# Kernel optimization log

Measured on AMD Instinct MI355X. Metric: run time of the kernel, lower is better.

Reference implementation:

```python
import jax, jax.numpy as jnp
import numpy as np

EMBED_DIM = 200
INPUT_DIM = 512


def setup_inputs() -> dict:
    key = jax.random.key(0)
    k1, k2, k3, k4 = jax.random.split(key, 4)
    B, L, T = 64, 256, 64
    x = jax.random.normal(k1, (B, L, INPUT_DIM), dtype=jnp.float32)
    y = jax.random.normal(k2, (B, T, INPUT_DIM), dtype=jnp.float32)
    # fc = nn.Linear(input_dim, embedding_dim)
    W = jax.random.normal(k3, (EMBED_DIM, INPUT_DIM), dtype=jnp.float32) * (1.0 / np.sqrt(INPUT_DIM))
    b = jax.random.normal(k4, (EMBED_DIM,), dtype=jnp.float32) * 0.01
    return {"x": x, "y": y, "W": W, "b": b}


def reference(x, y, W, b):
    # Project both modalities (last dim != embedding_dim in original triggers fc)
    xp = jnp.einsum('bld,ed->ble', x, W) + b   # B x L x E
    yp = jnp.einsum('btd,ed->bte', y, W) + b   # B x T x E
    # Pairwise matchmap: for pair (i, j), matchmap = xp[i] @ yp[j].T -> L x T
    mm = jnp.einsum('ile,jte->ijlt', xp, yp)   # B x B x L x T
    # MISA: max over L (rows of matchmap, dim 0), then mean over T
    S = jnp.max(mm, axis=2).mean(axis=2)       # B x B
    return S
```

## Files before the change

### kernel.cpp

```cpp
#include <hip/hip_runtime.h>
#include <hip/hip_bf16.h>
#include <stdint.h>

#define BB 64
#define LL 256
#define TT 64
#define DD 512
#define EE 200
#define EP 208
#define NKK 13
#define NROWS_X 16384
#define BSTRIDE 264

typedef __attribute__((ext_vector_type(8))) short short8;
typedef __attribute__((ext_vector_type(4))) float floatx4;
typedef __attribute__((ext_vector_type(16))) float floatx16;

__device__ __forceinline__ short f2bf(float f) {
  uint32_t u = __builtin_bit_cast(uint32_t, f);
  u = (u + 0x7fffu + ((u >> 16) & 1u)) >> 16;
  return (short)u;
}

__device__ __forceinline__ uint32_t pack2(float lo, float hi) {
  return __builtin_amdgcn_perm(__builtin_bit_cast(uint32_t, hi),
                               __builtin_bit_cast(uint32_t, lo), 0x07060302u);
}

typedef const __attribute__((address_space(1))) uint32_t gu32_t;
typedef __attribute__((address_space(3))) uint32_t lu32_t;
__device__ __forceinline__ void glds16(const void* g, void* l) {
  __builtin_amdgcn_global_load_lds((gu32_t*)g, (lu32_t*)l, 16, 0, 0);
}

__global__ void wcvt_kernel(const float* __restrict__ W, short* __restrict__ Wb) {
  const int t = blockIdx.x * 256 + threadIdx.x;
  const int base = t * 8;
  const int e = base >> 9;
  short8 o;
  if (e < EE) {
    const floatx4 f0 = *(const floatx4*)(W + base);
    const floatx4 f1 = *(const floatx4*)(W + base + 4);
    o[0] = f2bf(f0.x); o[1] = f2bf(f0.y); o[2] = f2bf(f0.z); o[3] = f2bf(f0.w);
    o[4] = f2bf(f1.x); o[5] = f2bf(f1.y); o[6] = f2bf(f1.z); o[7] = f2bf(f1.w);
  } else {
    o = (short8)0;
  }
  *(short8*)(Wb + base) = o;
}

__global__ __launch_bounds__(256, 3) void proj_kernel(const float* __restrict__ x,
                                                      const float* __restrict__ y,
                                                      const short* __restrict__ Wb,
                                                      const float* __restrict__ bias,
                                                      short* __restrict__ pT) {
  __shared__ __align__(16) char smem[43008];
  float* ldsA = (float*)smem;
  short* ldsB = (short*)(smem + 16384);
  short* bounce = (short*)smem;

  const int tid  = threadIdx.x;
  const int lane = tid & 63;
  const int wid  = tid >> 6;
  const int r16   = lane & 15;
  const int khalf = lane >> 4;

  const int row0 = blockIdx.x * 64;
  const float* srcbase = (row0 < NROWS_X) ? (x + (size_t)row0 * DD)
                                          : (y + (size_t)(row0 - NROWS_X) * DD);

  floatx4 acc[NKK];
#pragma unroll
  for (int n = 0; n < NKK; n++) acc[n] = (floatx4){0.f, 0.f, 0.f, 0.f};

  auto stage = [&](int buf, int ks) {
#pragma unroll
    for (int it = 0; it < 2; it++) {
      const int p = it * 256 + tid;
      const int r = p >> 3, c = p & 7;
      glds16(srcbase + (size_t)r * DD + ks * 32 + ((c ^ (r & 7)) << 2),
             &ldsA[buf * 2048 + p * 4]);
    }
#pragma unroll
    for (int it = 0; it < 4; it++) {
      const int p = it * 256 + tid;
      if (p < 832) {
        const int r = p >> 2, c = p & 3;
        glds16(Wb + (size_t)r * DD + ks * 32 + ((c ^ (r & 3)) << 3),
               &ldsB[buf * 6656 + p * 8]);
      }
    }
  };

  stage(0, 0);

  for (int s = 0; s < 16; s++) {
    __syncthreads();
    if (s + 1 < 16) stage((s + 1) & 1, s + 1);

    const int buf = s & 1;
    const int r = wid * 16 + r16;
    const int c0 = (2 * khalf) ^ (r & 7);
    const int c1 = (2 * khalf + 1) ^ (r & 7);
    const floatx4 f0 = *(const floatx4*)&ldsA[buf * 2048 + r * 32 + c0 * 4];
    const floatx4 f1 = *(const floatx4*)&ldsA[buf * 2048 + r * 32 + c1 * 4];
    union { short8 s8; uint32_t u[4]; } af;
    af.u[0] = pack2(f0.x, f0.y);
    af.u[1] = pack2(f0.z, f0.w);
    af.u[2] = pack2(f1.x, f1.y);
    af.u[3] = pack2(f1.z, f1.w);
#pragma unroll
    for (int n = 0; n < NKK; n++) {
      const int erow = n * 16 + r16;
      const short8 bfrag = *(const short8*)&ldsB[buf * 6656 + erow * 32 + ((khalf ^ (erow & 3)) << 3)];
      acc[n] = __builtin_amdgcn_mfma_f32_16x16x32_bf16(af.s8, bfrag, acc[n], 0, 0, 0);
    }
  }

  __syncthreads();

#pragma unroll
  for (int n = 0; n < NKK; n++) {
    const int e = n * 16 + r16;
    const float bv = (e < EE) ? bias[e] : 0.0f;
#pragma unroll
    for (int rr = 0; rr < 4; rr++) {
      const int lr = wid * 16 + khalf * 4 + rr;
      bounce[lr * BSTRIDE + e] = f2bf(acc[n][rr] + bv);
    }
  }
  __syncthreads();

  const int rowblk0 = row0 >> 5;
  for (int c = tid; c < 1664; c += 256) {
    const int q  = c >> 6;
    const int mt = (q >= 13) ? 1 : 0;
    const int n  = q - mt * 13;
    const int l  = c & 63;
    const int lr = mt * 32 + (l & 31);
    const short8 piece = *(const short8*)&bounce[lr * BSTRIDE + n * 16 + (l >> 5) * 8];
    *(short8*)&pT[((size_t)((rowblk0 + mt) * 13 + n)) * 512 + l * 8] = piece;
  }
}

__global__ __launch_bounds__(1024, 4) void pair_kernel(const short* __restrict__ xpT,
                                                       const short* __restrict__ ypT,
                                                       float* __restrict__ S) {
  __shared__ __align__(16) char lds[163840];
  short* Alds = (short*)lds;
  float* red  = (float*)(lds + 106496 + 53248);

  const int tid  = threadIdx.x;
  const int lane = tid & 63;
  const int wid  = tid >> 6;
  const int lt   = wid >> 1;
  const int nt   = wid & 1;
  const int bid  = blockIdx.x;
  const int i    = bid & 63;
  const int jq   = bid >> 6;
  const int jbase = jq * 16;

  {
    const short* src = xpT + (size_t)i * 104 * 512;
    for (int c = tid; c < 6656; c += 1024)
      glds16(src + (size_t)c * 8, lds + c * 16);
  }
  {
    const short* src = ypT + (size_t)jbase * 26 * 512;
    for (int c = tid; c < 1664; c += 1024)
      glds16(src + (size_t)c * 8, lds + 106496 + c * 16);
  }
  __syncthreads();

  const short* amine = Alds + (size_t)(lt * NKK) * 512 + lane * 8;

  for (int jj = 0; jj < 16; jj++) {
    const int buf = jj & 1;

    if (jj + 1 < 16) {
      const short* src = ypT + (size_t)(jbase + jj + 1) * 26 * 512;
      char* dst = lds + 106496 + (buf ^ 1) * 26624;
      for (int c = tid; c < 1664; c += 1024)
        glds16(src + (size_t)c * 8, dst + c * 16);
    }

    floatx16 acc;
#pragma unroll
    for (int r = 0; r < 16; r++) acc[r] = 0.f;
    const short* bmine = (short*)(lds + 106496 + buf * 26624) + (size_t)(nt * NKK) * 512 + lane * 8;
#pragma unroll
    for (int kk = 0; kk < NKK; kk++) {
      const short8 a = *(const short8*)(amine + kk * 512);
      const short8 b = *(const short8*)(bmine + kk * 512);
      acc = __builtin_amdgcn_mfma_f32_32x32x16_bf16(a, b, acc, 0, 0, 0);
    }

    float v = acc[0];
#pragma unroll
    for (int r = 1; r < 16; r++) v = fmaxf(v, acc[r]);
    v = fmaxf(v, __shfl_xor(v, 32, 64));
    if (lane < 32)
      red[(buf * 8 + lt) * 64 + nt * 32 + lane] = v;

    __syncthreads();

    if (wid == jj) {
      float m = red[(buf * 8 + 0) * 64 + lane];
#pragma unroll
      for (int l2 = 1; l2 < 8; l2++)
        m = fmaxf(m, red[(buf * 8 + l2) * 64 + lane]);
      m += __shfl_xor(m, 1, 64);
      m += __shfl_xor(m, 2, 64);
      m += __shfl_xor(m, 4, 64);
      m += __shfl_xor(m, 8, 64);
      m += __shfl_xor(m, 16, 64);
      m += __shfl_xor(m, 32, 64);
      if (lane == 0) S[i * BB + jbase + jj] = m * (1.0f / 64.0f);
    }
  }
}

extern "C" void kernel_launch(void* const* d_in, const int* in_sizes, int n_in,
                              void* d_out, int out_size, void* d_ws, size_t ws_size,
                              hipStream_t stream) {
  const float* x = (const float*)d_in[0];
  const float* y = (const float*)d_in[1];
  const float* W = (const float*)d_in[2];
  const float* b = (const float*)d_in[3];
  float* S = (float*)d_out;

  char* ws = (char*)d_ws;
  short* Wb = (short*)ws;
  short* pT = (short*)(ws + 262144);
  short* ypT = pT + (size_t)6656 * 512;

  wcvt_kernel<<<52, 256, 0, stream>>>(W, Wb);
  proj_kernel<<<320, 256, 0, stream>>>(x, y, Wb, b, pT);
  pair_kernel<<<256, 1024, 0, stream>>>(pT, ypT, S);
}
```

Measured before the change: 52.54 us.

## Hold x-projection fragments in registers and compute 2x2 MFMA tiles per wave

The pair kernel no longer stages the xp block in LDS. Each wave now keeps two 32-row L tiles of A fragments in registers and computes a 2x2 tile of 32x32 MFMA outputs per step, so every LDS B fragment is reused twice. The block shrinks to 512 threads and processes two j values per iteration, with the final reduction deferred until after the loop, which cuts the number of barriers. The cost is much higher register pressure (26 short8 A fragments plus four floatx16 accumulators), which may lower occupancy.

After: 47.92 us. -8.8%, faster.

```diff
diff --git a/kernel.cpp b/kernel.cpp
--- a/kernel.cpp
+++ b/kernel.cpp
@@ -143,80 +143,97 @@
   }
 }
 
-__global__ __launch_bounds__(1024, 4) void pair_kernel(const short* __restrict__ xpT,
-                                                       const short* __restrict__ ypT,
-                                                       float* __restrict__ S) {
-  __shared__ __align__(16) char lds[163840];
-  short* Alds = (short*)lds;
-  float* red  = (float*)(lds + 106496 + 53248);
+__global__ __launch_bounds__(512, 2) void pair_kernel(const short* __restrict__ xpT,
+                                                      const short* __restrict__ ypT,
+                                                      float* __restrict__ S) {
+  __shared__ __align__(16) char lds[2 * 53248 + 16384];
+  float* red = (float*)(lds + 2 * 53248);
 
   const int tid  = threadIdx.x;
   const int lane = tid & 63;
   const int wid  = tid >> 6;
-  const int lt   = wid >> 1;
-  const int nt   = wid & 1;
+  const int jj2  = wid >> 2;
+  const int wj   = wid & 3;
   const int bid  = blockIdx.x;
   const int i    = bid & 63;
   const int jq   = bid >> 6;
   const int jbase = jq * 16;
 
+  short8 a0[NKK], a1[NKK];
   {
-    const short* src = xpT + (size_t)i * 104 * 512;
-    for (int c = tid; c < 6656; c += 1024)
-      glds16(src + (size_t)c * 8, lds + c * 16);
-  }
-  {
-    const short* src = ypT + (size_t)jbase * 26 * 512;
-    for (int c = tid; c < 1664; c += 1024)
-      glds16(src + (size_t)c * 8, lds + 106496 + c * 16);
-  }
+    const short* ab0 = xpT + ((size_t)((i * 8 + wj * 2 + 0) * NKK)) * 512 + lane * 8;
+    const short* ab1 = xpT + ((size_t)((i * 8 + wj * 2 + 1) * NKK)) * 512 + lane * 8;
+#pragma unroll
+    for (int kk = 0; kk < NKK; kk++) {
+      a0[kk] = *(const short8*)(ab0 + kk * 512);
+      a1[kk] = *(const short8*)(ab1 + kk * 512);
+    }
+  }
+
+  auto stageB = [&](int g) {
+    const short* src = ypT + (size_t)(jbase + g * 2) * 26 * 512;
+    char* dst = lds + (g & 1) * 53248;
+    for (int c = tid; c < 3328; c += 512)
+      glds16(src + (size_t)c * 8, dst + c * 16);
+  };
+
+  stageB(0);
   __syncthreads();
 
-  const short* amine = Alds + (size_t)(lt * NKK) * 512 + lane * 8;
-
-  for (int jj = 0; jj < 16; jj++) {
-    const int buf = jj & 1;
-
-    if (jj + 1 < 16) {
-      const short* src = ypT + (size_t)(jbase + jj + 1) * 26 * 512;
-      char* dst = lds + 106496 + (buf ^ 1) * 26624;
-      for (int c = tid; c < 1664; c += 1024)
-        glds16(src + (size_t)c * 8, dst + c * 16);
-    }
-
-    floatx16 acc;
-#pragma unroll
-    for (int r = 0; r < 16; r++) acc[r] = 0.f;
-    const short* bmine = (short*)(lds + 106496 + buf * 26624) + (size_t)(nt * NKK) * 512 + lane * 8;
+  for (int g = 0; g < 8; g++) {
+    if (g + 1 < 8) stageB(g + 1);
+
+    const int j = g * 2 + jj2;
+    const short* bbase = (const short*)(lds + (g & 1) * 53248) +
+                         (size_t)(jj2 * 26 * 512) + lane * 8;
+
+    floatx16 accA0n0, accA0n1, accA1n0, accA1n1;
+#pragma unroll
+    for (int r = 0; r < 16; r++) {
+      accA0n0[r] = 0.f; accA0n1[r] = 0.f; accA1n0[r] = 0.f; accA1n1[r] = 0.f;
+    }
+
 #pragma unroll
     for (int kk = 0; kk < NKK; kk++) {
-      const short8 a = *(const short8*)(amine + kk * 512);
-      const short8 b = *(const short8*)(bmine + kk * 512);
-      acc = __builtin_amdgcn_mfma_f32_32x32x16_bf16(a, b, acc, 0, 0, 0);
-    }
-
-    float v = acc[0];
-#pragma unroll
-    for (int r = 1; r < 16; r++) v = fmaxf(v, acc[r]);
-    v = fmaxf(v, __shfl_xor(v, 32, 64));
-    if (lane < 32)
-      red[(buf * 8 + lt) * 64 + nt * 32 + lane] = v;
+      const short8 b0 = *(const short8*)(bbase + (0 * NKK + kk) * 512);
+      const short8 b1 = *(const short8*)(bbase + (1 * NKK + kk) * 512);
+      accA0n0 = __builtin_amdgcn_mfma_f32_32x32x16_bf16(a0[kk], b0, accA0n0, 0, 0, 0);
+      accA1n0 = __builtin_amdgcn_mfma_f32_32x32x16_bf16(a1[kk], b0, accA1n0, 0, 0, 0);
+      accA0n1 = __builtin_amdgcn_mfma_f32_32x32x16_bf16(a0[kk], b1, accA0n1, 0, 0, 0);
+      accA1n1 = __builtin_amdgcn_mfma_f32_32x32x16_bf16(a1[kk], b1, accA1n1, 0, 0, 0);
+    }
+
+    float v0 = accA0n0[0], v1 = accA0n1[0];
+#pragma unroll
+    for (int r = 0; r < 16; r++) {
+      v0 = fmaxf(v0, accA0n0[r]); v0 = fmaxf(v0, accA1n0[r]);
+      v1 = fmaxf(v1, accA0n1[r]); v1 = fmaxf(v1, accA1n1[r]);
+    }
+    v0 = fmaxf(v0, __shfl_xor(v0, 32, 64));
+    v1 = fmaxf(v1, __shfl_xor(v1, 32, 64));
+    if (lane < 32) {
+      red[(j * 4 + wj) * 64 + 0 * 32 + lane] = v0;
+      red[(j * 4 + wj) * 64 + 1 * 32 + lane] = v1;
+    }
 
     __syncthreads();
-
-    if (wid == jj) {
-      float m = red[(buf * 8 + 0) * 64 + lane];
-#pragma unroll
-      for (int l2 = 1; l2 < 8; l2++)
-        m = fmaxf(m, red[(buf * 8 + l2) * 64 + lane]);
-      m += __shfl_xor(m, 1, 64);
-      m += __shfl_xor(m, 2, 64);
-      m += __shfl_xor(m, 4, 64);
-      m += __shfl_xor(m, 8, 64);
-      m += __shfl_xor(m, 16, 64);
-      m += __shfl_xor(m, 32, 64);
-      if (lane == 0) S[i * BB + jbase + jj] = m * (1.0f / 64.0f);
-    }
+  }
+
+#pragma unroll
+  for (int rep = 0; rep < 2; rep++) {
+    const int j = wid * 2 + rep;
+    const int t = lane;
+    float v = red[(j * 4 + 0) * 64 + t];
+    v = fmaxf(v, red[(j * 4 + 1) * 64 + t]);
+    v = fmaxf(v, red[(j * 4 + 2) * 64 + t]);
+    v = fmaxf(v, red[(j * 4 + 3) * 64 + t]);
+    v += __shfl_xor(v, 1, 64);
+    v += __shfl_xor(v, 2, 64);
+    v += __shfl_xor(v, 4, 64);
+    v += __shfl_xor(v, 8, 64);
+    v += __shfl_xor(v, 16, 64);
+    v += __shfl_xor(v, 32, 64);
+    if (t == 0) S[i * BB + jbase + j] = v * (1.0f / 64.0f);
   }
 }
 
@@ -236,5 +253,5 @@
 
   wcvt_kernel<<<52, 256, 0, stream>>>(W, Wb);
   proj_kernel<<<320, 256, 0, stream>>>(x, y, Wb, b, pT);
-  pair_kernel<<<256, 1024, 0, stream>>>(pT, ypT, S);
-}
+  pair_kernel<<<256, 512, 0, stream>>>(pT, ypT, S);
+}
```
